# Optimization experiments

Hardware: AMD Instinct MI355X
Metric: run time of the kernel (lower is better)

Reference implementation:

```python
import jax, jax.numpy as jnp
import numpy as np

EMBED = 1024
HEADS = 16
HEAD_DIM = EMBED // HEADS


def setup_inputs() -> dict:
    key = jax.random.key(0)
    ks = jax.random.split(key, 7)
    B, S = 4, 2048
    q = jax.random.normal(ks[0], (B, S, EMBED), dtype=jnp.float32)
    k = jax.random.normal(ks[1], (B, S, EMBED), dtype=jnp.float32)
    v = jax.random.normal(ks[2], (B, S, EMBED), dtype=jnp.float32)
    # causal mask, broadcast over heads: [B, 1, S, S]
    mask = jnp.broadcast_to(jnp.tril(jnp.ones((S, S), dtype=jnp.int32))[None, None], (B, 1, S, S))
    scale = 1.0 / np.sqrt(EMBED)
    w_q = jax.random.normal(ks[3], (EMBED, EMBED), dtype=jnp.float32) * scale
    w_k = jax.random.normal(ks[4], (EMBED, EMBED), dtype=jnp.float32) * scale
    w_v = jax.random.normal(ks[5], (EMBED, EMBED), dtype=jnp.float32) * scale
    w_o = jax.random.normal(ks[6], (EMBED, EMBED), dtype=jnp.float32) * scale
    return {"q": q, "k": k, "v": v, "mask": mask,
            "w_q": w_q, "w_k": w_k, "w_v": w_v, "w_o": w_o}


def reference(q, k, v, mask, w_q, w_k, w_v, w_o):
    B, S, _ = q.shape
    # Linear projections (torch Linear: x @ W^T), split into heads: [B,H,S,D]
    def proj(x, w):
        return (x @ w.T).reshape(B, -1, HEADS, HEAD_DIM).transpose(0, 2, 1, 3)
    qh, kh, vh = proj(q, w_q), proj(k, w_k), proj(v, w_v)
    scores = jnp.einsum('bhqd,bhkd->bhqk', qh, kh) / jnp.sqrt(jnp.float32(HEAD_DIM))
    scores = jnp.where(mask == 0, jnp.float32(-1e9), scores)
    attn = jax.nn.softmax(scores, axis=-1)
    # dropout is identity in eval/reference mode
    x = jnp.einsum('bhqk,bhkd->bhqd', attn, vh)  # [B,H,S,D]
    x = x.transpose(0, 2, 1, 3).reshape(B, S, HEADS * HEAD_DIM)
    return x @ w_o.T
```

## Files before the change

kernel.cpp:

```cpp
#include <hip/hip_runtime.h>

typedef unsigned short u16;
typedef __attribute__((ext_vector_type(8))) short v8s;
typedef __attribute__((ext_vector_type(4))) float v4f;

#define S_LEN  2048
#define NHEADS 16
#define DHEAD  64
#define EMB    1024

#if __has_builtin(__builtin_amdgcn_exp2f)
#define EXP2F __builtin_amdgcn_exp2f
#else
#define EXP2F exp2f
#endif

__device__ __forceinline__ u16 f32_bf16(float f) {
  union { float f; unsigned u; } x; x.f = f;
  unsigned r = x.u + 0x7fffu + ((x.u >> 16) & 1u);
  return (u16)(r >> 16);
}

__device__ __forceinline__ void async16(const void* g, void* l) {
  __builtin_amdgcn_global_load_lds(
      (const __attribute__((address_space(1))) unsigned int*)g,
      (__attribute__((address_space(3))) unsigned int*)l, 16, 0, 0);
}

__global__ __launch_bounds__(256) void cvt_all(
    const float4* __restrict__ s0, const float4* __restrict__ s1,
    const float4* __restrict__ s2, const float4* __restrict__ s3,
    const float4* __restrict__ s4, const float4* __restrict__ s5,
    const float4* __restrict__ s6,
    ushort4* __restrict__ d0, ushort4* __restrict__ d1,
    ushort4* __restrict__ d2, ushort4* __restrict__ d3,
    ushort4* __restrict__ d4, ushort4* __restrict__ d5,
    ushort4* __restrict__ d6, int nbig, int nsmall) {
  const int y = blockIdx.y;
  const float4* s; ushort4* d;
  switch (y) {
    case 0: s = s0; d = d0; break;  case 1: s = s1; d = d1; break;
    case 2: s = s2; d = d2; break;  case 3: s = s3; d = d3; break;
    case 4: s = s4; d = d4; break;  case 5: s = s5; d = d5; break;
    default: s = s6; d = d6; break;
  }
  const int n4 = (y < 3) ? nbig : nsmall;
  for (int i = blockIdx.x * 256 + threadIdx.x; i < n4; i += gridDim.x * 256) {
    const float4 v = s[i];
    ushort4 o;
    o.x = f32_bf16(v.x); o.y = f32_bf16(v.y);
    o.z = f32_bf16(v.z); o.w = f32_bf16(v.w);
    d[i] = o;
  }
}

__global__ __launch_bounds__(256) void gemm_qkv(const u16* __restrict__ A,
                                                const u16* __restrict__ W0,
                                                const u16* __restrict__ W1,
                                                const u16* __restrict__ W2,
                                                u16* __restrict__ Cq,
                                                u16* __restrict__ Ck,
                                                u16* __restrict__ Cv) {
  __shared__ __align__(16) u16 lA[128 * 32];
  __shared__ __align__(16) u16 lB[128 * 32];
  const int K = EMB;
  const int t = threadIdx.x;
  const int lane = t & 63, w = t >> 6;
  const int m0 = blockIdx.x << 7, n0 = blockIdx.y << 7;
  const int sec = m0 >> 13;
  const u16* W = (sec == 0) ? W0 : ((sec == 1) ? W1 : W2);
  u16* C = (sec == 0) ? Cq : ((sec == 1) ? Ck : Cv);
  const int wm = (w >> 1) << 6, wn = (w & 1) << 6;
  const int qr = lane >> 4, cl = lane & 15;

  v4f acc[4][4];
#pragma unroll
  for (int i = 0; i < 4; ++i)
#pragma unroll
    for (int j = 0; j < 4; ++j) acc[i][j] = (v4f){0.f, 0.f, 0.f, 0.f};

  for (int kt = 0; kt < (K >> 5); ++kt) {
    const int k0 = kt << 5;
    __syncthreads();
#pragma unroll
    for (int i = 0; i < 2; ++i) {
      const int c = t + (i << 8);
      async16(A + (size_t)(m0 + (c >> 2)) * K + k0 + ((c & 3) << 3),
              &lA[(w * 64 + i * 256) * 8]);
      async16(W + (size_t)(n0 + (c >> 2)) * K + k0 + ((c & 3) << 3),
              &lB[(w * 64 + i * 256) * 8]);
    }
    __syncthreads();
    v8s af[4], bf[4];
#pragma unroll
    for (int mi = 0; mi < 4; ++mi)
      af[mi] = *(const v8s*)&lA[(wm + mi * 16 + cl) * 32 + qr * 8];
#pragma unroll
    for (int ni = 0; ni < 4; ++ni)
      bf[ni] = *(const v8s*)&lB[(wn + ni * 16 + cl) * 32 + qr * 8];
#pragma unroll
    for (int mi = 0; mi < 4; ++mi)
#pragma unroll
      for (int ni = 0; ni < 4; ++ni)
        acc[mi][ni] = __builtin_amdgcn_mfma_f32_16x16x32_bf16(af[mi], bf[ni],
                                                              acc[mi][ni], 0, 0, 0);
  }

#pragma unroll
  for (int mi = 0; mi < 4; ++mi)
#pragma unroll
    for (int ni = 0; ni < 4; ++ni)
#pragma unroll
      for (int r = 0; r < 4; ++r) {
        const int mloc = (m0 & 8191) + wm + mi * 16 + qr * 4 + r;
        const int n = n0 + wn + ni * 16 + cl;
        const int b = mloc >> 11, s = mloc & (S_LEN - 1);
        const int h = n >> 6, d = n & (DHEAD - 1);
        const size_t idx = (sec < 2)
            ? (((size_t)b * NHEADS + h) * S_LEN + s) * DHEAD + d
            : (((size_t)b * NHEADS + h) * DHEAD + d) * S_LEN + s;
        C[idx] = f32_bf16(acc[mi][ni][r]);
      }
}

__global__ __launch_bounds__(256) void gemm_out(const u16* __restrict__ A,
                                                const u16* __restrict__ W,
                                                float* __restrict__ C,
                                                int M, int N, int K) {
  __shared__ __align__(16) u16 lA[128 * 32];
  __shared__ __align__(16) u16 lB[128 * 32];
  const int t = threadIdx.x;
  const int lane = t & 63, w = t >> 6;
  const int m0 = blockIdx.x << 7, n0 = blockIdx.y << 7;
  const int wm = (w >> 1) << 6, wn = (w & 1) << 6;
  const int qr = lane >> 4, cl = lane & 15;

  v4f acc[4][4];
#pragma unroll
  for (int i = 0; i < 4; ++i)
#pragma unroll
    for (int j = 0; j < 4; ++j) acc[i][j] = (v4f){0.f, 0.f, 0.f, 0.f};

  for (int kt = 0; kt < (K >> 5); ++kt) {
    const int k0 = kt << 5;
    __syncthreads();
#pragma unroll
    for (int i = 0; i < 2; ++i) {
      const int c = t + (i << 8);
      async16(A + (size_t)(m0 + (c >> 2)) * K + k0 + ((c & 3) << 3),
              &lA[(w * 64 + i * 256) * 8]);
      async16(W + (size_t)(n0 + (c >> 2)) * K + k0 + ((c & 3) << 3),
              &lB[(w * 64 + i * 256) * 8]);
    }
    __syncthreads();
    v8s af[4], bf[4];
#pragma unroll
    for (int mi = 0; mi < 4; ++mi)
      af[mi] = *(const v8s*)&lA[(wm + mi * 16 + cl) * 32 + qr * 8];
#pragma unroll
    for (int ni = 0; ni < 4; ++ni)
      bf[ni] = *(const v8s*)&lB[(wn + ni * 16 + cl) * 32 + qr * 8];
#pragma unroll
    for (int mi = 0; mi < 4; ++mi)
#pragma unroll
      for (int ni = 0; ni < 4; ++ni)
        acc[mi][ni] = __builtin_amdgcn_mfma_f32_16x16x32_bf16(af[mi], bf[ni],
                                                              acc[mi][ni], 0, 0, 0);
  }

#pragma unroll
  for (int mi = 0; mi < 4; ++mi)
#pragma unroll
    for (int ni = 0; ni < 4; ++ni)
#pragma unroll
      for (int r = 0; r < 4; ++r) {
        const int m = m0 + wm + mi * 16 + qr * 4 + r;
        const int n = n0 + wn + ni * 16 + cl;
        C[(size_t)m * N + n] = acc[mi][ni][r];
      }
}

__global__ __launch_bounds__(256) void attn_causal(const u16* __restrict__ Qp,
                                                   const u16* __restrict__ Kp,
                                                   const u16* __restrict__ VpT,
                                                   u16* __restrict__ Out) {
  __shared__ __align__(16) u16 lK[2][64 * 64];
  __shared__ __align__(16) u16 lV[2][64 * 64];
  __shared__ __align__(16) u16 pb[4][32 * 64];
  const int t = threadIdx.x;
  const int lane = t & 63, w = t >> 6;
  const int qr = lane >> 4, cl = lane & 15;
  const int id = blockIdx.x;
  const int col = (id & 7) + (((id >> 3) >> 4) << 3);
  const int qt = 15 - ((id >> 3) & 15);
  const int h = col & 15, b = col >> 4;
  const int q0 = qt << 7;
  const size_t bh = ((size_t)b * NHEADS + h) * S_LEN * DHEAD;
  const u16* Qb = Qp + bh;
  const u16* Kb = Kp + bh;
  const u16* Vb = VpT + bh;

  const int wr0 = q0 + w * 32;
  v8s aq[2][2];
#pragma unroll
  for (int mf = 0; mf < 2; ++mf)
#pragma unroll
    for (int kf = 0; kf < 2; ++kf)
      aq[mf][kf] = *(const v8s*)(Qb + (size_t)(wr0 + mf * 16 + cl) * DHEAD +
                                 kf * 32 + qr * 8);

  v4f o[2][4], lac[2];
#pragma unroll
  for (int mf = 0; mf < 2; ++mf) {
    lac[mf] = (v4f){0.f, 0.f, 0.f, 0.f};
#pragma unroll
    for (int nf = 0; nf < 4; ++nf) o[mf][nf] = (v4f){0.f, 0.f, 0.f, 0.f};
  }
  v8s vone;
#pragma unroll
  for (int j = 0; j < 8; ++j) vone[j] = (short)0x3F80;

  const float SC = 0.125f * 1.4426950408889634f;
  const int nkt = 2 * qt + 2;

#pragma unroll
  for (int i = 0; i < 2; ++i) {
    const int c = t + (i << 8);
    const int krow = c >> 3, kdc = (c & 7) ^ (krow & 7);
    async16(Kb + (size_t)krow * DHEAD + kdc * 8, &lK[0][(w * 64 + (i << 8)) * 8]);
    const int vd = c >> 3, vkc = (c & 7) ^ (vd & 7);
    async16(Vb + (size_t)vd * S_LEN + vkc * 8, &lV[0][(w * 64 + (i << 8)) * 8]);
  }

  for (int kt = 0; kt < nkt; ++kt) {
    const int k0 = kt << 6;
    const int cb = kt & 1;
    __syncthreads();
    if (kt + 1 < nkt) {
      const int kn = (kt + 1) << 6;
#pragma unroll
      for (int i = 0; i < 2; ++i) {
        const int c = t + (i << 8);
        const int krow = c >> 3, kdc = (c & 7) ^ (krow & 7);
        async16(Kb + (size_t)(kn + krow) * DHEAD + kdc * 8,
                &lK[1 - cb][(w * 64 + (i << 8)) * 8]);
        const int vd = c >> 3, vkc = (c & 7) ^ (vd & 7);
        async16(Vb + (size_t)vd * S_LEN + kn + vkc * 8,
                &lV[1 - cb][(w * 64 + (i << 8)) * 8]);
      }
    }
    if (k0 > wr0 + 31) continue;

    v4f sacc[2][4];
#pragma unroll
    for (int mf = 0; mf < 2; ++mf)
#pragma unroll
      for (int ni = 0; ni < 4; ++ni) sacc[mf][ni] = (v4f){0.f, 0.f, 0.f, 0.f};
#pragma unroll
    for (int kf = 0; kf < 2; ++kf)
#pragma unroll
      for (int ni = 0; ni < 4; ++ni) {
        const v8s bk = *(const v8s*)&lK[cb][((ni * 16 + cl) * 8 +
                                            (((kf << 2) + qr) ^ (cl & 7))) * 8];
        sacc[0][ni] = __builtin_amdgcn_mfma_f32_16x16x32_bf16(aq[0][kf], bk,
                                                              sacc[0][ni], 0, 0, 0);
        sacc[1][ni] = __builtin_amdgcn_mfma_f32_16x16x32_bf16(aq[1][kf], bk,
                                                              sacc[1][ni], 0, 0, 0);
      }

#pragma unroll
    for (int mf = 0; mf < 2; ++mf) {
      const int rowb0 = wr0 + mf * 16;
      if (k0 + 63 <= rowb0) {
#pragma unroll
        for (int ni = 0; ni < 4; ++ni) {
          const int kc = ni * 2 + (cl >> 3);
#pragma unroll
          for (int r = 0; r < 4; ++r) {
            const float e = EXP2F(sacc[mf][ni][r] * SC);
            pb[w][((kc * 32 + mf * 16 + r * 4 + qr) << 3) + (cl & 7)] =
                (u16)(__float_as_uint(e) >> 16);
          }
        }
      } else {
        const int rowb = rowb0 + qr * 4;
#pragma unroll
        for (int ni = 0; ni < 4; ++ni) {
          const int colk = k0 + ni * 16 + cl;
          const int kc = ni * 2 + (cl >> 3);
#pragma unroll
          for (int r = 0; r < 4; ++r) {
            float e = EXP2F(sacc[mf][ni][r] * SC);
            if (colk > rowb + r) e = 0.f;
            pb[w][((kc * 32 + mf * 16 + r * 4 + qr) << 3) + (cl & 7)] =
                (u16)(__float_as_uint(e) >> 16);
          }
        }
      }
    }

#pragma unroll
    for (int kf = 0; kf < 2; ++kf) {
      const int kc = (kf << 2) + qr;
      const int sig0 = ((cl & 3) << 2) + (cl >> 2);
      const v8s ap0 = *(const v8s*)&pb[w][((kc * 32 + sig0) << 3)];
      const v8s ap1 = *(const v8s*)&pb[w][((kc * 32 + 16 + sig0) << 3)];
      lac[0] = __builtin_amdgcn_mfma_f32_16x16x32_bf16(ap0, vone, lac[0], 0, 0, 0);
      lac[1] = __builtin_amdgcn_mfma_f32_16x16x32_bf16(ap1, vone, lac[1], 0, 0, 0);
#pragma unroll
      for (int nf = 0; nf < 4; ++nf) {
        const v8s bv = *(const v8s*)&lV[cb][((nf * 16 + cl) * 8 +
                                            (kc ^ (cl & 7))) * 8];
        o[0][nf] = __builtin_amdgcn_mfma_f32_16x16x32_bf16(ap0, bv, o[0][nf], 0, 0, 0);
        o[1][nf] = __builtin_amdgcn_mfma_f32_16x16x32_bf16(ap1, bv, o[1][nf], 0, 0, 0);
      }
    }
  }

#pragma unroll
  for (int mf = 0; mf < 2; ++mf) {
    float inv[4];
#pragma unroll
    for (int r = 0; r < 4; ++r) inv[r] = 1.0f / lac[mf][r];
#pragma unroll
    for (int nf = 0; nf < 4; ++nf)
#pragma unroll
      for (int r = 0; r < 4; ++r) {
        const int row = wr0 + mf * 16 + qr * 4 + r;
        const int colo = h * DHEAD + nf * 16 + cl;
        Out[((size_t)b * S_LEN + row) * EMB + colo] = f32_bf16(o[mf][nf][r] * inv[r]);
      }
  }
}

extern "C" void kernel_launch(void* const* d_in, const int* in_sizes, int n_in,
                              void* d_out, int out_size, void* d_ws, size_t ws_size,
                              hipStream_t stream) {
  (void)in_sizes; (void)n_in; (void)out_size; (void)ws_size;
  const float* q  = (const float*)d_in[0];
  const float* k  = (const float*)d_in[1];
  const float* v  = (const float*)d_in[2];
  const float* wq = (const float*)d_in[4];
  const float* wk = (const float*)d_in[5];
  const float* wv = (const float*)d_in[6];
  const float* wo = (const float*)d_in[7];
  float* out = (float*)d_out;

  const size_t MT = (size_t)4 * S_LEN * EMB;
  const size_t WT = (size_t)EMB * EMB;
  u16* p = (u16*)d_ws;
  u16* xq = p; p += MT;
  u16* xk = p; p += MT;
  u16* xv = p; p += MT;
  u16* wqb = p; p += WT;
  u16* wkb = p; p += WT;
  u16* wvb = p; p += WT;
  u16* wob = p; p += WT;
  u16* Qp = p; p += MT;
  u16* Kp = p; p += MT;
  u16* Vp = p; p += MT;
  u16* Ao = xq;

  const dim3 blk(256);
  hipLaunchKernelGGL(cvt_all, dim3(512, 7), blk, 0, stream,
                     (const float4*)q, (const float4*)k, (const float4*)v,
                     (const float4*)wq, (const float4*)wk, (const float4*)wv,
                     (const float4*)wo,
                     (ushort4*)xq, (ushort4*)xk, (ushort4*)xv,
                     (ushort4*)wqb, (ushort4*)wkb, (ushort4*)wvb, (ushort4*)wob,
                     (int)(MT / 4), (int)(WT / 4));
  hipLaunchKernelGGL(gemm_qkv, dim3(192, 8), blk, 0, stream,
                     xq, wqb, wkb, wvb, Qp, Kp, Vp);
  hipLaunchKernelGGL(attn_causal, dim3(1024), blk, 0, stream, Qp, Kp, Vp, Ao);
  hipLaunchKernelGGL(gemm_out, dim3(64, 8), blk, 0, stream, Ao, wob, out,
                     8192, 1024, 1024);
}
```

Measured before the change: 388.5 us.

## Double-buffer GEMM LDS tiles and pair causal query tiles per attention block

Both projection GEMMs now use two LDS buffers and prefetch the next K-tile with async loads before computing the current one. This removes one barrier per iteration and overlaps global-to-LDS traffic with MFMA work. The attention kernel now launches half as many blocks, and each block processes a long and a short causal query tile (15-p and p), so every block gets a similar amount of work. The GEMM change doubles LDS use per block, which may lower occupancy. The pairing cuts parallelism to 512 blocks and serialises two phases per block.

```diff
diff --git a/kernel.cpp b/kernel.cpp
--- a/kernel.cpp
+++ b/kernel.cpp
@@ -61,8 +61,8 @@
                                                 u16* __restrict__ Cq,
                                                 u16* __restrict__ Ck,
                                                 u16* __restrict__ Cv) {
-  __shared__ __align__(16) u16 lA[128 * 32];
-  __shared__ __align__(16) u16 lB[128 * 32];
+  __shared__ __align__(16) u16 lA[2][128 * 32];
+  __shared__ __align__(16) u16 lB[2][128 * 32];
   const int K = EMB;
   const int t = threadIdx.x;
   const int lane = t & 63, w = t >> 6;
@@ -79,25 +79,37 @@
 #pragma unroll
     for (int j = 0; j < 4; ++j) acc[i][j] = (v4f){0.f, 0.f, 0.f, 0.f};
 
-  for (int kt = 0; kt < (K >> 5); ++kt) {
-    const int k0 = kt << 5;
+#pragma unroll
+  for (int i = 0; i < 2; ++i) {
+    const int c = t + (i << 8);
+    async16(A + (size_t)(m0 + (c >> 2)) * K + ((c & 3) << 3),
+            &lA[0][(w * 64 + i * 256) * 8]);
+    async16(W + (size_t)(n0 + (c >> 2)) * K + ((c & 3) << 3),
+            &lB[0][(w * 64 + i * 256) * 8]);
+  }
+
+  const int nk = K >> 5;
+  for (int kt = 0; kt < nk; ++kt) {
+    const int cb = kt & 1;
     __syncthreads();
-#pragma unroll
-    for (int i = 0; i < 2; ++i) {
-      const int c = t + (i << 8);
-      async16(A + (size_t)(m0 + (c >> 2)) * K + k0 + ((c & 3) << 3),
-              &lA[(w * 64 + i * 256) * 8]);
-      async16(W + (size_t)(n0 + (c >> 2)) * K + k0 + ((c & 3) << 3),
-              &lB[(w * 64 + i * 256) * 8]);
-    }
-    __syncthreads();
+    if (kt + 1 < nk) {
+      const int kn = (kt + 1) << 5;
+#pragma unroll
+      for (int i = 0; i < 2; ++i) {
+        const int c = t + (i << 8);
+        async16(A + (size_t)(m0 + (c >> 2)) * K + kn + ((c & 3) << 3),
+                &lA[1 - cb][(w * 64 + i * 256) * 8]);
+        async16(W + (size_t)(n0 + (c >> 2)) * K + kn + ((c & 3) << 3),
+                &lB[1 - cb][(w * 64 + i * 256) * 8]);
+      }
+    }
     v8s af[4], bf[4];
 #pragma unroll
     for (int mi = 0; mi < 4; ++mi)
-      af[mi] = *(const v8s*)&lA[(wm + mi * 16 + cl) * 32 + qr * 8];
+      af[mi] = *(const v8s*)&lA[cb][(wm + mi * 16 + cl) * 32 + qr * 8];
 #pragma unroll
     for (int ni = 0; ni < 4; ++ni)
-      bf[ni] = *(const v8s*)&lB[(wn + ni * 16 + cl) * 32 + qr * 8];
+      bf[ni] = *(const v8s*)&lB[cb][(wn + ni * 16 + cl) * 32 + qr * 8];
 #pragma unroll
     for (int mi = 0; mi < 4; ++mi)
 #pragma unroll
@@ -127,8 +139,8 @@
                                                 const u16* __restrict__ W,
                                                 float* __restrict__ C,
                                                 int M, int N, int K) {
-  __shared__ __align__(16) u16 lA[128 * 32];
-  __shared__ __align__(16) u16 lB[128 * 32];
+  __shared__ __align__(16) u16 lA[2][128 * 32];
+  __shared__ __align__(16) u16 lB[2][128 * 32];
   const int t = threadIdx.x;
   const int lane = t & 63, w = t >> 6;
   const int m0 = blockIdx.x << 7, n0 = blockIdx.y << 7;
@@ -141,25 +153,37 @@
 #pragma unroll
     for (int j = 0; j < 4; ++j) acc[i][j] = (v4f){0.f, 0.f, 0.f, 0.f};
 
-  for (int kt = 0; kt < (K >> 5); ++kt) {
-    const int k0 = kt << 5;
+#pragma unroll
+  for (int i = 0; i < 2; ++i) {
+    const int c = t + (i << 8);
+    async16(A + (size_t)(m0 + (c >> 2)) * K + ((c & 3) << 3),
+            &lA[0][(w * 64 + i * 256) * 8]);
+    async16(W + (size_t)(n0 + (c >> 2)) * K + ((c & 3) << 3),
+            &lB[0][(w * 64 + i * 256) * 8]);
+  }
+
+  const int nk = K >> 5;
+  for (int kt = 0; kt < nk; ++kt) {
+    const int cb = kt & 1;
     __syncthreads();
-#pragma unroll
-    for (int i = 0; i < 2; ++i) {
-      const int c = t + (i << 8);
-      async16(A + (size_t)(m0 + (c >> 2)) * K + k0 + ((c & 3) << 3),
-              &lA[(w * 64 + i * 256) * 8]);
-      async16(W + (size_t)(n0 + (c >> 2)) * K + k0 + ((c & 3) << 3),
-              &lB[(w * 64 + i * 256) * 8]);
-    }
-    __syncthreads();
+    if (kt + 1 < nk) {
+      const int kn = (kt + 1) << 5;
+#pragma unroll
+      for (int i = 0; i < 2; ++i) {
+        const int c = t + (i << 8);
+        async16(A + (size_t)(m0 + (c >> 2)) * K + kn + ((c & 3) << 3),
+                &lA[1 - cb][(w * 64 + i * 256) * 8]);
+        async16(W + (size_t)(n0 + (c >> 2)) * K + kn + ((c & 3) << 3),
+                &lB[1 - cb][(w * 64 + i * 256) * 8]);
+      }
+    }
     v8s af[4], bf[4];
 #pragma unroll
     for (int mi = 0; mi < 4; ++mi)
-      af[mi] = *(const v8s*)&lA[(wm + mi * 16 + cl) * 32 + qr * 8];
+      af[mi] = *(const v8s*)&lA[cb][(wm + mi * 16 + cl) * 32 + qr * 8];
 #pragma unroll
     for (int ni = 0; ni < 4; ++ni)
-      bf[ni] = *(const v8s*)&lB[(wn + ni * 16 + cl) * 32 + qr * 8];
+      bf[ni] = *(const v8s*)&lB[cb][(wn + ni * 16 + cl) * 32 + qr * 8];
 #pragma unroll
     for (int mi = 0; mi < 4; ++mi)
 #pragma unroll
@@ -191,145 +215,150 @@
   const int lane = t & 63, w = t >> 6;
   const int qr = lane >> 4, cl = lane & 15;
   const int id = blockIdx.x;
-  const int col = (id & 7) + (((id >> 3) >> 4) << 3);
-  const int qt = 15 - ((id >> 3) & 15);
+  const int col = (id & 7) + ((id >> 6) << 3);
+  const int pair = (id >> 3) & 7;
   const int h = col & 15, b = col >> 4;
-  const int q0 = qt << 7;
   const size_t bh = ((size_t)b * NHEADS + h) * S_LEN * DHEAD;
   const u16* Qb = Qp + bh;
   const u16* Kb = Kp + bh;
   const u16* Vb = VpT + bh;
 
-  const int wr0 = q0 + w * 32;
-  v8s aq[2][2];
-#pragma unroll
-  for (int mf = 0; mf < 2; ++mf)
-#pragma unroll
-    for (int kf = 0; kf < 2; ++kf)
-      aq[mf][kf] = *(const v8s*)(Qb + (size_t)(wr0 + mf * 16 + cl) * DHEAD +
-                                 kf * 32 + qr * 8);
-
-  v4f o[2][4], lac[2];
-#pragma unroll
-  for (int mf = 0; mf < 2; ++mf) {
-    lac[mf] = (v4f){0.f, 0.f, 0.f, 0.f};
-#pragma unroll
-    for (int nf = 0; nf < 4; ++nf) o[mf][nf] = (v4f){0.f, 0.f, 0.f, 0.f};
-  }
   v8s vone;
 #pragma unroll
   for (int j = 0; j < 8; ++j) vone[j] = (short)0x3F80;
-
   const float SC = 0.125f * 1.4426950408889634f;
-  const int nkt = 2 * qt + 2;
-
-#pragma unroll
-  for (int i = 0; i < 2; ++i) {
-    const int c = t + (i << 8);
-    const int krow = c >> 3, kdc = (c & 7) ^ (krow & 7);
-    async16(Kb + (size_t)krow * DHEAD + kdc * 8, &lK[0][(w * 64 + (i << 8)) * 8]);
-    const int vd = c >> 3, vkc = (c & 7) ^ (vd & 7);
-    async16(Vb + (size_t)vd * S_LEN + vkc * 8, &lV[0][(w * 64 + (i << 8)) * 8]);
-  }
-
-  for (int kt = 0; kt < nkt; ++kt) {
-    const int k0 = kt << 6;
-    const int cb = kt & 1;
+
+  for (int phase = 0; phase < 2; ++phase) {
+    const int qt = phase == 0 ? (15 - pair) : pair;
+    const int q0 = qt << 7;
+    const int wr0 = q0 + w * 32;
+
+    v8s aq[2][2];
+#pragma unroll
+    for (int mf = 0; mf < 2; ++mf)
+#pragma unroll
+      for (int kf = 0; kf < 2; ++kf)
+        aq[mf][kf] = *(const v8s*)(Qb + (size_t)(wr0 + mf * 16 + cl) * DHEAD +
+                                   kf * 32 + qr * 8);
+
+    v4f o[2][4], lac[2];
+#pragma unroll
+    for (int mf = 0; mf < 2; ++mf) {
+      lac[mf] = (v4f){0.f, 0.f, 0.f, 0.f};
+#pragma unroll
+      for (int nf = 0; nf < 4; ++nf) o[mf][nf] = (v4f){0.f, 0.f, 0.f, 0.f};
+    }
+
+    const int nkt = 2 * qt + 2;
     __syncthreads();
-    if (kt + 1 < nkt) {
-      const int kn = (kt + 1) << 6;
-#pragma unroll
-      for (int i = 0; i < 2; ++i) {
-        const int c = t + (i << 8);
-        const int krow = c >> 3, kdc = (c & 7) ^ (krow & 7);
-        async16(Kb + (size_t)(kn + krow) * DHEAD + kdc * 8,
-                &lK[1 - cb][(w * 64 + (i << 8)) * 8]);
-        const int vd = c >> 3, vkc = (c & 7) ^ (vd & 7);
-        async16(Vb + (size_t)vd * S_LEN + kn + vkc * 8,
-                &lV[1 - cb][(w * 64 + (i << 8)) * 8]);
-      }
-    }
-    if (k0 > wr0 + 31) continue;
-
-    v4f sacc[2][4];
-#pragma unroll
-    for (int mf = 0; mf < 2; ++mf)
-#pragma unroll
-      for (int ni = 0; ni < 4; ++ni) sacc[mf][ni] = (v4f){0.f, 0.f, 0.f, 0.f};
-#pragma unroll
-    for (int kf = 0; kf < 2; ++kf)
-#pragma unroll
-      for (int ni = 0; ni < 4; ++ni) {
-        const v8s bk = *(const v8s*)&lK[cb][((ni * 16 + cl) * 8 +
-                                            (((kf << 2) + qr) ^ (cl & 7))) * 8];
-        sacc[0][ni] = __builtin_amdgcn_mfma_f32_16x16x32_bf16(aq[0][kf], bk,
-                                                              sacc[0][ni], 0, 0, 0);
-        sacc[1][ni] = __builtin_amdgcn_mfma_f32_16x16x32_bf16(aq[1][kf], bk,
-                                                              sacc[1][ni], 0, 0, 0);
-      }
-
-#pragma unroll
-    for (int mf = 0; mf < 2; ++mf) {
-      const int rowb0 = wr0 + mf * 16;
-      if (k0 + 63 <= rowb0) {
+#pragma unroll
+    for (int i = 0; i < 2; ++i) {
+      const int c = t + (i << 8);
+      const int krow = c >> 3, kdc = (c & 7) ^ (krow & 7);
+      async16(Kb + (size_t)krow * DHEAD + kdc * 8, &lK[0][(w * 64 + (i << 8)) * 8]);
+      const int vd = c >> 3, vkc = (c & 7) ^ (vd & 7);
+      async16(Vb + (size_t)vd * S_LEN + vkc * 8, &lV[0][(w * 64 + (i << 8)) * 8]);
+    }
+
+    for (int kt = 0; kt < nkt; ++kt) {
+      const int k0 = kt << 6;
+      const int cb = kt & 1;
+      __syncthreads();
+      if (kt + 1 < nkt) {
+        const int kn = (kt + 1) << 6;
+#pragma unroll
+        for (int i = 0; i < 2; ++i) {
+          const int c = t + (i << 8);
+          const int krow = c >> 3, kdc = (c & 7) ^ (krow & 7);
+          async16(Kb + (size_t)(kn + krow) * DHEAD + kdc * 8,
+                  &lK[1 - cb][(w * 64 + (i << 8)) * 8]);
+          const int vd = c >> 3, vkc = (c & 7) ^ (vd & 7);
+          async16(Vb + (size_t)vd * S_LEN + kn + vkc * 8,
+                  &lV[1 - cb][(w * 64 + (i << 8)) * 8]);
+        }
+      }
+      if (k0 > wr0 + 31) continue;
+
+      v4f sacc[2][4];
+#pragma unroll
+      for (int mf = 0; mf < 2; ++mf)
+#pragma unroll
+        for (int ni = 0; ni < 4; ++ni) sacc[mf][ni] = (v4f){0.f, 0.f, 0.f, 0.f};
+#pragma unroll
+      for (int kf = 0; kf < 2; ++kf)
 #pragma unroll
         for (int ni = 0; ni < 4; ++ni) {
-          const int kc = ni * 2 + (cl >> 3);
-#pragma unroll
-          for (int r = 0; r < 4; ++r) {
-            const float e = EXP2F(sacc[mf][ni][r] * SC);
-            pb[w][((kc * 32 + mf * 16 + r * 4 + qr) << 3) + (cl & 7)] =
-                (u16)(__float_as_uint(e) >> 16);
+          const v8s bk = *(const v8s*)&lK[cb][((ni * 16 + cl) * 8 +
+                                              (((kf << 2) + qr) ^ (cl & 7))) * 8];
+          sacc[0][ni] = __builtin_amdgcn_mfma_f32_16x16x32_bf16(aq[0][kf], bk,
+                                                                sacc[0][ni], 0, 0, 0);
+          sacc[1][ni] = __builtin_amdgcn_mfma_f32_16x16x32_bf16(aq[1][kf], bk,
+                                                                sacc[1][ni], 0, 0, 0);
+        }
+
+#pragma unroll
+      for (int mf = 0; mf < 2; ++mf) {
+        const int rowb0 = wr0 + mf * 16;
+        if (k0 + 63 <= rowb0) {
+#pragma unroll
+          for (int ni = 0; ni < 4; ++ni) {
+            const int kc = ni * 2 + (cl >> 3);
+#pragma unroll
+            for (int r = 0; r < 4; ++r) {
+              const float e = EXP2F(sacc[mf][ni][r] * SC);
+              pb[w][((kc * 32 + mf * 16 + r * 4 + qr) << 3) + (cl & 7)] =
+                  (u16)(__float_as_uint(e) >> 16);
+            }
+          }
+        } else {
+          const int rowb = rowb0 + qr * 4;
+#pragma unroll
+          for (int ni = 0; ni < 4; ++ni) {
+            const int colk = k0 + ni * 16 + cl;
+            const int kc = ni * 2 + (cl >> 3);
+#pragma unroll
+            for (int r = 0; r < 4; ++r) {
+              float e = EXP2F(sacc[mf][ni][r] * SC);
+              if (colk > rowb + r) e = 0.f;
+              pb[w][((kc * 32 + mf * 16 + r * 4 + qr) << 3) + (cl & 7)] =
+                  (u16)(__float_as_uint(e) >> 16);
+            }
           }
         }
-      } else {
-        const int rowb = rowb0 + qr * 4;
-#pragma unroll
-        for (int ni = 0; ni < 4; ++ni) {
-          const int colk = k0 + ni * 16 + cl;
-          const int kc = ni * 2 + (cl >> 3);
-#pragma unroll
-          for (int r = 0; r < 4; ++r) {
-            float e = EXP2F(sacc[mf][ni][r] * SC);
-            if (colk > rowb + r) e = 0.f;
-            pb[w][((kc * 32 + mf * 16 + r * 4 + qr) << 3) + (cl & 7)] =
-                (u16)(__float_as_uint(e) >> 16);
-          }
+      }
+
+#pragma unroll
+      for (int kf = 0; kf < 2; ++kf) {
+        const int kc = (kf << 2) + qr;
+        const int sig0 = ((cl & 3) << 2) + (cl >> 2);
+        const v8s ap0 = *(const v8s*)&pb[w][((kc * 32 + sig0) << 3)];
+        const v8s ap1 = *(const v8s*)&pb[w][((kc * 32 + 16 + sig0) << 3)];
+        lac[0] = __builtin_amdgcn_mfma_f32_16x16x32_bf16(ap0, vone, lac[0], 0, 0, 0);
+        lac[1] = __builtin_amdgcn_mfma_f32_16x16x32_bf16(ap1, vone, lac[1], 0, 0, 0);
+#pragma unroll
+        for (int nf = 0; nf < 4; ++nf) {
+          const v8s bv = *(const v8s*)&lV[cb][((nf * 16 + cl) * 8 +
+                                              (kc ^ (cl & 7))) * 8];
+          o[0][nf] = __builtin_amdgcn_mfma_f32_16x16x32_bf16(ap0, bv, o[0][nf], 0, 0, 0);
+          o[1][nf] = __builtin_amdgcn_mfma_f32_16x16x32_bf16(ap1, bv, o[1][nf], 0, 0, 0);
         }
       }
     }
 
 #pragma unroll
-    for (int kf = 0; kf < 2; ++kf) {
-      const int kc = (kf << 2) + qr;
-      const int sig0 = ((cl & 3) << 2) + (cl >> 2);
-      const v8s ap0 = *(const v8s*)&pb[w][((kc * 32 + sig0) << 3)];
-      const v8s ap1 = *(const v8s*)&pb[w][((kc * 32 + 16 + sig0) << 3)];
-      lac[0] = __builtin_amdgcn_mfma_f32_16x16x32_bf16(ap0, vone, lac[0], 0, 0, 0);
-      lac[1] = __builtin_amdgcn_mfma_f32_16x16x32_bf16(ap1, vone, lac[1], 0, 0, 0);
-#pragma unroll
-      for (int nf = 0; nf < 4; ++nf) {
-        const v8s bv = *(const v8s*)&lV[cb][((nf * 16 + cl) * 8 +
-                                            (kc ^ (cl & 7))) * 8];
-        o[0][nf] = __builtin_amdgcn_mfma_f32_16x16x32_bf16(ap0, bv, o[0][nf], 0, 0, 0);
-        o[1][nf] = __builtin_amdgcn_mfma_f32_16x16x32_bf16(ap1, bv, o[1][nf], 0, 0, 0);
-      }
-    }
-  }
-
-#pragma unroll
-  for (int mf = 0; mf < 2; ++mf) {
-    float inv[4];
-#pragma unroll
-    for (int r = 0; r < 4; ++r) inv[r] = 1.0f / lac[mf][r];
-#pragma unroll
-    for (int nf = 0; nf < 4; ++nf)
-#pragma unroll
-      for (int r = 0; r < 4; ++r) {
-        const int row = wr0 + mf * 16 + qr * 4 + r;
-        const int colo = h * DHEAD + nf * 16 + cl;
-        Out[((size_t)b * S_LEN + row) * EMB + colo] = f32_bf16(o[mf][nf][r] * inv[r]);
-      }
+    for (int mf = 0; mf < 2; ++mf) {
+      float inv[4];
+#pragma unroll
+      for (int r = 0; r < 4; ++r) inv[r] = 1.0f / lac[mf][r];
+#pragma unroll
+      for (int nf = 0; nf < 4; ++nf)
+#pragma unroll
+        for (int r = 0; r < 4; ++r) {
+          const int row = wr0 + mf * 16 + qr * 4 + r;
+          const int colo = h * DHEAD + nf * 16 + cl;
+          Out[((size_t)b * S_LEN + row) * EMB + colo] = f32_bf16(o[mf][nf][r] * inv[r]);
+        }
+    }
   }
 }
 
@@ -371,7 +400,7 @@
                      (int)(MT / 4), (int)(WT / 4));
   hipLaunchKernelGGL(gemm_qkv, dim3(192, 8), blk, 0, stream,
                      xq, wqb, wkb, wvb, Qp, Kp, Vp);
-  hipLaunchKernelGGL(attn_causal, dim3(1024), blk, 0, stream, Qp, Kp, Vp, Ao);
+  hipLaunchKernelGGL(attn_causal, dim3(512), blk, 0, stream, Qp, Kp, Vp, Ao);
   hipLaunchKernelGGL(gemm_out, dim3(64, 8), blk, 0, stream, Ao, wob, out,
                      8192, 1024, 1024);
 }
```

Result: faster. 365.5 us (-5.9%).
